# Performance work log

Measured on AMD Instinct MI355X. Metric: run time of the kernel, lower is better.

Reference implementation:

```python
import jax, jax.numpy as jnp
import numpy as np

N = 8192
IN_F = 512
OUT_F = 512
ALPHA = 0.2  # LeakyReLU negative slope
MASK_VAL = -9e15


def setup_inputs() -> dict:
    key = jax.random.key(0)
    k1, k2, k3, k4 = jax.random.split(key, 4)
    h = jax.random.normal(k1, (N, IN_F), dtype=jnp.float32)
    adj = jax.random.randint(k2, (N, N), 0, 2, dtype=jnp.int32)
    # Xavier-uniform-like init for params
    limW = float(1.414 * np.sqrt(6.0 / (IN_F + OUT_F)))
    W = jax.random.uniform(k3, (IN_F, OUT_F), dtype=jnp.float32, minval=-limW, maxval=limW)
    lima = float(1.414 * np.sqrt(6.0 / (2 * OUT_F + 1)))
    a = jax.random.uniform(k4, (2 * OUT_F, 1), dtype=jnp.float32, minval=-lima, maxval=lima)
    return {"h": h, "adj": adj, "W": W, "a": a}


def reference(h, adj, W, a):
    Wh = h @ W                                   # [N, F_out]
    a1 = a[:OUT_F, 0]                            # [F_out]
    a2 = a[OUT_F:, 0]                            # [F_out]
    # e_ij = leakyrelu(Wh_i . a1 + Wh_j . a2), broadcast sum instead of concat
    e = jax.nn.leaky_relu((Wh @ a1)[:, None] + (Wh @ a2)[None, :], negative_slope=ALPHA)
    attention = jnp.where(adj > 0, e, MASK_VAL)  # [N, N]
    attention = jax.nn.softmax(attention, axis=1)
    similarity = attention                       # softmax=True branch
    h_prime = attention @ Wh                     # [N, F_out]
    return jax.nn.elu(h_prime), similarity       # concat=True branch
```

## Files before the change

### kernel.cpp

```cpp
#include <hip/hip_runtime.h>
#include <stdint.h>
#include <stddef.h>

#define NN 8192
#define FD 512
#define ATTN_OFF (NN * FD)

typedef __attribute__((ext_vector_type(8))) short bf16x8;
typedef __attribute__((ext_vector_type(4))) float f32x4;
typedef __attribute__((ext_vector_type(4))) int i32x4;
typedef __attribute__((ext_vector_type(2))) uint32_t u32x2;
typedef __attribute__((ext_vector_type(4))) uint32_t u32x4;
typedef __attribute__((ext_vector_type(4))) uint16_t u16x4;

static __device__ __forceinline__ uint16_t f2bf(float x){
    union { float f; uint32_t u; } v; v.f = x;
    uint32_t r = v.u + 0x7FFFu + ((v.u >> 16) & 1u);
    return (uint16_t)(r >> 16);
}

#define GLDS(gp, lp) \
    __builtin_amdgcn_global_load_lds((__attribute__((address_space(1))) void*)(gp), \
                                     (__attribute__((address_space(3))) void*)(lp), 16, 0, 0)

__global__ void k_va(const float* __restrict__ W, const float* __restrict__ a,
                     float* __restrict__ va1, float* __restrict__ va2){
    const int lane = threadIdx.x & 63, wave = threadIdx.x >> 6;
    const int k = blockIdx.x*8 + wave;
    const float* wr = W + (size_t)k*FD;
    float s1 = 0.f, s2 = 0.f;
    #pragma unroll
    for (int e = 0; e < 2; ++e){
        int c = e*256 + lane*4;
        f32x4 wv = *(const f32x4*)(wr + c);
        f32x4 x1 = *(const f32x4*)(a + c);
        f32x4 x2 = *(const f32x4*)(a + FD + c);
        s1 += wv[0]*x1[0] + wv[1]*x1[1] + wv[2]*x1[2] + wv[3]*x1[3];
        s2 += wv[0]*x2[0] + wv[1]*x2[1] + wv[2]*x2[2] + wv[3]*x2[3];
    }
    for (int off = 32; off; off >>= 1){ s1 += __shfl_down(s1, off); s2 += __shfl_down(s2, off); }
    if (lane == 0){ va1[k] = s1; va2[k] = s2; }
}

__global__ void k_convW(const float* __restrict__ W, uint16_t* __restrict__ WT_b){
    int idx = blockIdx.x * 256 + threadIdx.x;
    for (int i = idx; i < FD*FD; i += 256*256){
        int n = i >> 9, k = i & 511;
        WT_b[i] = f2bf(W[(size_t)k*FD + n]);
    }
}

__global__ void k_rows(const float* __restrict__ h, const float* __restrict__ va1,
                       const float* __restrict__ va2, uint16_t* __restrict__ h_b,
                       float* __restrict__ Tarr,
                       float* __restrict__ E1p, float* __restrict__ E1n,
                       float* __restrict__ E2p, float* __restrict__ E2n){
    const int lane = threadIdx.x & 63, wave = threadIdx.x >> 6;
    const int row = blockIdx.x*4 + wave;
    const float* hr = h + (size_t)row * FD;
    float s1 = 0.f, s2 = 0.f;
    #pragma unroll
    for (int e = 0; e < 2; ++e){
        int c = e*256 + lane*4;
        f32x4 hv = *(const f32x4*)(hr + c);
        f32x4 x1 = *(const f32x4*)(va1 + c);
        f32x4 x2 = *(const f32x4*)(va2 + c);
        s1 += hv[0]*x1[0] + hv[1]*x1[1] + hv[2]*x1[2] + hv[3]*x1[3];
        s2 += hv[0]*x2[0] + hv[1]*x2[1] + hv[2]*x2[2] + hv[3]*x2[3];
        u16x4 o;
        o[0]=f2bf(hv[0]); o[1]=f2bf(hv[1]); o[2]=f2bf(hv[2]); o[3]=f2bf(hv[3]);
        *(u16x4*)(h_b + (size_t)row*FD + c) = o;
    }
    for (int off = 32; off; off >>= 1){ s1 += __shfl_down(s1, off); s2 += __shfl_down(s2, off); }
    if (lane == 0){
        Tarr[row] = expf(-s1);
        E1p[row]  = expf(s1);
        E1n[row]  = expf(0.2f*s1);
        E2p[row]  = expf(s2);
        E2n[row]  = expf(0.2f*s2);
    }
}

__global__ void k_pack(const int* __restrict__ adj, const float* __restrict__ Tarr,
                       const float* __restrict__ E1p, const float* __restrict__ E1n,
                       const float* __restrict__ E2p, const float* __restrict__ E2n,
                       uint32_t* __restrict__ packed, float* __restrict__ rowP,
                       float* __restrict__ rowN){
    extern __shared__ char smem[];
    float* P_s = (float*)smem;
    float* Q_s = (float*)(smem + 32768);
    const int tid = threadIdx.x, lane = tid & 63, wave = tid >> 6;
    for (int t = tid; t < NN/4; t += 256){
        ((f32x4*)P_s)[t] = ((const f32x4*)E2p)[t];
        ((f32x4*)Q_s)[t] = ((const f32x4*)E2n)[t];
    }
    __syncthreads();
    const int row = blockIdx.x*4 + wave;
    const float T_i = Tarr[row];
    const int* arow = adj + (size_t)row * NN;
    float Ap = 0.f, An = 0.f;
    #pragma unroll
    for (int g = 0; g < 4; ++g){
        uint32_t word = 0;
        #pragma unroll
        for (int e = 0; e < 8; ++e){
            int j0 = g*2048 + e*256 + lane*4;
            i32x4 av = __builtin_nontemporal_load((const i32x4*)(arow + j0));
            f32x4 p = ((const f32x4*)P_s)[j0 >> 2];
            f32x4 q = ((const f32x4*)Q_s)[j0 >> 2];
            #pragma unroll
            for (int c = 0; c < 4; ++c){
                if (av[c] != 0){
                    if (p[c] > T_i) Ap += p[c]; else An += q[c];
                    word |= (1u << (e*4 + c));
                }
            }
        }
        packed[(size_t)row*256 + g*64 + lane] = word;
    }
    #pragma unroll
    for (int off = 32; off; off >>= 1){
        Ap += __shfl_xor(Ap, off);
        An += __shfl_xor(An, off);
    }
    if (lane == 0){
        float e1p = E1p[row], e1n = E1n[row];
        float inv = 1.0f / (e1p*Ap + e1n*An);
        rowP[row] = e1p * inv;
        rowN[row] = e1n * inv;
    }
}

static __device__ __forceinline__ void mfma_tile(const char* A_base, const char* B_base,
                                                 int wave, int lane, f32x4 acc[2][4]){
    #pragma unroll
    for (int kk = 0; kk < 2; ++kk){
        bf16x8 afr[2], bfr[4];
        #pragma unroll
        for (int t = 0; t < 2; ++t){
            int rowl = t*16 + (lane & 15);
            int slot = (kk*4 + (lane >> 4)) ^ (rowl & 7);
            afr[t] = *(const bf16x8*)(A_base + rowl*128 + slot*16);
        }
        #pragma unroll
        for (int n = 0; n < 4; ++n){
            int nl = wave*64 + n*16 + (lane & 15);
            int slot = (kk*4 + (lane >> 4)) ^ (nl & 7);
            bfr[n] = *(const bf16x8*)(B_base + nl*128 + slot*16);
        }
        #pragma unroll
        for (int t = 0; t < 2; ++t)
            #pragma unroll
            for (int n = 0; n < 4; ++n)
                acc[t][n] = __builtin_amdgcn_mfma_f32_16x16x32_bf16(afr[t], bfr[n], acc[t][n], 0, 0, 0);
    }
}

__global__ __launch_bounds__(512) void k_wh(const uint16_t* __restrict__ h_b,
                                            const uint16_t* __restrict__ WT_b,
                                            uint16_t* __restrict__ WhbT){
    extern __shared__ char smem[];
    char* A_base = smem;
    char* B_base = smem + 4096;
    const int tid = threadIdx.x, wave = tid >> 6, lane = tid & 63;
    const int mb0 = blockIdx.x * 32;
    f32x4 acc[2][4];
    #pragma unroll
    for (int t = 0; t < 2; ++t)
        #pragma unroll
        for (int n = 0; n < 4; ++n) acc[t][n] = (f32x4){0.f,0.f,0.f,0.f};

    for (int k0 = 0; k0 < FD; k0 += 64){
        if (wave < 4){
            int m = wave*8 + (lane >> 3);
            int chunk = (lane & 7) ^ (m & 7);
            GLDS(h_b + (size_t)(mb0 + m)*FD + k0 + chunk*8, A_base + wave*1024);
        }
        #pragma unroll
        for (int r = 0; r < 8; ++r){
            int nn = wave*64 + r*8 + (lane >> 3);
            int chunk = (lane & 7) ^ (nn & 7);
            GLDS(WT_b + (size_t)nn*FD + k0 + chunk*8, B_base + (wave*64 + r*8)*128);
        }
        __syncthreads();
        mfma_tile(A_base, B_base, wave, lane, acc);
        __syncthreads();
    }
    uint16_t* Ts = (uint16_t*)B_base;
    #pragma unroll
    for (int t = 0; t < 2; ++t)
        #pragma unroll
        for (int n = 0; n < 4; ++n)
            #pragma unroll
            for (int r = 0; r < 4; ++r){
                int nl = wave*64 + n*16 + (lane & 15);
                int m  = t*16 + (lane >> 4)*4 + r;
                Ts[nl*40 + m] = f2bf(acc[t][n][r]);
            }
    __syncthreads();
    {
        int n = tid;
        const u32x4* src = (const u32x4*)(Ts + n*40);
        u32x4* dst = (u32x4*)(WhbT + (size_t)n*NN + mb0);
        #pragma unroll
        for (int r = 0; r < 4; ++r) dst[r] = src[r];
    }
}

__global__ __launch_bounds__(512) void k_gemm(const uint32_t* __restrict__ packed,
                                              const uint16_t* __restrict__ WhbT,
                                              const float* __restrict__ Tarr,
                                              const float* __restrict__ rowP,
                                              const float* __restrict__ rowN,
                                              const float* __restrict__ E2p,
                                              const float* __restrict__ E2n,
                                              float* __restrict__ hp_part,
                                              float* __restrict__ out){
    extern __shared__ char smem[];
    char* A_lds = smem;
    char* B_lds = smem + 16384;

    const int tid = threadIdx.x, wave = tid >> 6, lane = tid & 63;
    const int il = tid >> 3, jg = tid & 7;
    const int bi = blockIdx.x;
    const int ks = (bi & 7) >> 1;
    const int m_idx = (bi >> 3)*2 + (bi & 1);
    const int row0 = m_idx * 128;
    const int kbase = ks * 2048;

    float Tv[2], rPv[2], rNv[2];
    #pragma unroll
    for (int s = 0; s < 2; ++s){
        int gr = row0 + il + 64*s;
        Tv[s] = Tarr[gr]; rPv[s] = rowP[gr]; rNv[s] = rowN[gr];
    }

    f32x4 acc[8][4];
    #pragma unroll
    for (int mi = 0; mi < 8; ++mi)
        #pragma unroll
        for (int n = 0; n < 4; ++n) acc[mi][n] = (f32x4){0.f,0.f,0.f,0.f};

    auto BLOAD = [&](int t, u32x4 br[4]){
        const int k0 = kbase + t*32;
        #pragma unroll
        for (int rr = 0; rr < 4; ++rr){
            int n  = wave*64 + rr*16 + (lane >> 2);
            int cg = lane & 3;
            br[rr] = *(const u32x4*)(WhbT + (size_t)n*NN + k0 + cg*8);
        }
    };
    auto GEN = [&](int t, uint32_t aw[2][2]){
        const int k0 = kbase + t*32;
        f32x4 p = *(const f32x4*)(E2p + k0 + jg*4);
        f32x4 q = *(const f32x4*)(E2n + k0 + jg*4);
        const int widx  = ks*64 + (t & 7)*8 + jg;
        const int shift = ((t >> 3) & 7)*4;
        #pragma unroll
        for (int s = 0; s < 2; ++s){
            int grow = row0 + il + 64*s;
            uint32_t word = packed[(size_t)grow*256 + widx];
            float va[4];
            #pragma unroll
            for (int c = 0; c < 4; ++c){
                float val = (p[c] > Tv[s]) ? rPv[s]*p[c] : rNv[s]*q[c];
                va[c] = ((word >> (shift + c)) & 1u) ? val : 0.f;
            }
            f32x4 st; st[0]=va[0]; st[1]=va[1]; st[2]=va[2]; st[3]=va[3];
            __builtin_nontemporal_store(st, (f32x4*)(out + ATTN_OFF + (size_t)grow*NN + k0 + jg*4));
            aw[s][0] = ((uint32_t)f2bf(va[1]) << 16) | f2bf(va[0]);
            aw[s][1] = ((uint32_t)f2bf(va[3]) << 16) | f2bf(va[2]);
        }
    };
    auto WRITE_LDS = [&](int side, uint32_t aw[2][2], u32x4 br[4]){
        char* A = A_lds + side*8192;
        char* B = B_lds + side*32768;
        #pragma unroll
        for (int s = 0; s < 2; ++s){
            int rowl = il + 64*s;
            int addr = rowl*64 + (((jg >> 1) ^ (rowl & 3)) << 4) + ((jg & 1) << 3);
            u32x2 w; w[0] = aw[s][0]; w[1] = aw[s][1];
            *(u32x2*)(A + addr) = w;
        }
        #pragma unroll
        for (int rr = 0; rr < 4; ++rr){
            int n  = wave*64 + rr*16 + (lane >> 2);
            int cg = lane & 3;
            *(u32x4*)(B + n*64 + ((cg ^ (n & 3)) << 4)) = br[rr];
        }
    };

    {
        uint32_t aw[2][2]; u32x4 br[4];
        BLOAD(0, br); GEN(0, aw);
        WRITE_LDS(0, aw, br);
        asm volatile("s_waitcnt lgkmcnt(0)" ::: "memory");
        __builtin_amdgcn_s_barrier();
    }

    for (int t = 0; t < 64; ++t){
        uint32_t aw[2][2]; u32x4 br[4];
        if (t < 63){ BLOAD(t+1, br); GEN(t+1, aw); }
        {
            const char* A = A_lds + (t & 1)*8192;
            const char* B = B_lds + (t & 1)*32768;
            bf16x8 afr[8], bfr[4];
            #pragma unroll
            for (int mi = 0; mi < 8; ++mi){
                int rowl = mi*16 + (lane & 15);
                afr[mi] = *(const bf16x8*)(A + rowl*64 + (((lane >> 4) ^ (rowl & 3)) << 4));
            }
            #pragma unroll
            for (int nf = 0; nf < 4; ++nf){
                int nl = wave*64 + nf*16 + (lane & 15);
                bfr[nf] = *(const bf16x8*)(B + nl*64 + (((lane >> 4) ^ (nl & 3)) << 4));
            }
            __builtin_amdgcn_s_setprio(1);
            #pragma unroll
            for (int mi = 0; mi < 8; ++mi)
                #pragma unroll
                for (int nf = 0; nf < 4; ++nf)
                    acc[mi][nf] = __builtin_amdgcn_mfma_f32_16x16x32_bf16(afr[mi], bfr[nf], acc[mi][nf], 0, 0, 0);
            __builtin_amdgcn_s_setprio(0);
        }
        if (t < 63){
            WRITE_LDS((t+1) & 1, aw, br);
            asm volatile("s_waitcnt lgkmcnt(0)" ::: "memory");
            __builtin_amdgcn_s_barrier();
        }
    }
    float* hp = hp_part + (size_t)ks * NN * FD;
    #pragma unroll
    for (int mi = 0; mi < 8; ++mi)
        #pragma unroll
        for (int n = 0; n < 4; ++n)
            #pragma unroll
            for (int r = 0; r < 4; ++r){
                int m   = row0 + mi*16 + (lane >> 4)*4 + r;
                int col = wave*64 + n*16 + (lane & 15);
                hp[(size_t)m*FD + col] = acc[mi][n][r];
            }
}

__global__ __launch_bounds__(512) void k_red(const float* __restrict__ hp,
                                             float* __restrict__ out){
    const size_t i = (size_t)blockIdx.x * 512 + threadIdx.x;
    const size_t off = (size_t)NN * FD / 4;
    f32x4 a = ((const f32x4*)hp)[i];
    f32x4 b = ((const f32x4*)hp)[i + off];
    f32x4 c = ((const f32x4*)hp)[i + off*2];
    f32x4 d = ((const f32x4*)hp)[i + off*3];
    f32x4 s;
    #pragma unroll
    for (int e = 0; e < 4; ++e){
        float x = (a[e] + b[e]) + (c[e] + d[e]);
        s[e] = (x > 0.f) ? x : expm1f(x);
    }
    ((f32x4*)out)[i] = s;
}

extern "C" void kernel_launch(void* const* d_in, const int* in_sizes, int n_in,
                              void* d_out, int out_size, void* d_ws, size_t ws_size,
                              hipStream_t stream){
    (void)in_sizes; (void)n_in; (void)out_size; (void)ws_size;
    const float* h   = (const float*)d_in[0];
    const int*   adj = (const int*)  d_in[1];
    const float* W   = (const float*)d_in[2];
    const float* a   = (const float*)d_in[3];
    float* out = (float*)d_out;

    char* ws = (char*)d_ws;
    uint16_t* WhbT   = (uint16_t*)(ws);
    uint16_t* h_b    = (uint16_t*)(ws + (8u<<20));
    uint32_t* packed = (uint32_t*)(ws + (8u<<20));
    uint16_t* WT_b   = (uint16_t*)(ws + (16u<<20));
    float* fb   = (float*)(ws + (17u<<20));
    float* va1  = fb;            float* va2  = fb + 512;
    float* Tarr = fb + 1024;
    float* E1p  = Tarr + NN;     float* E1n  = E1p + NN;
    float* E2p  = E1n + NN;      float* E2n  = E2p + NN;
    float* rowP = E2n + NN;      float* rowN = rowP + NN;
    float* hp_part = (float*)(ws + (32u<<20));

    hipFuncSetAttribute((const void*)k_pack, hipFuncAttributeMaxDynamicSharedMemorySize, 65536);
    hipFuncSetAttribute((const void*)k_wh,   hipFuncAttributeMaxDynamicSharedMemorySize, 69632);
    hipFuncSetAttribute((const void*)k_gemm, hipFuncAttributeMaxDynamicSharedMemorySize, 81920);

    k_va   <<<64,   512, 0,      stream>>>(W, a, va1, va2);
    k_rows <<<2048, 256, 0,      stream>>>(h, va1, va2, h_b, Tarr, E1p, E1n, E2p, E2n);
    k_convW<<<256,  256, 0,      stream>>>(W, WT_b);
    k_wh   <<<256,  512, 69632,  stream>>>(h_b, WT_b, WhbT);
    k_pack <<<2048, 256, 65536,  stream>>>(adj, Tarr, E1p, E1n, E2p, E2n, packed, rowP, rowN);
    k_gemm <<<256,  512, 81920,  stream>>>(packed, WhbT, Tarr, rowP, rowN, E2p, E2n, hp_part, out);
    k_red  <<<2048, 512, 0,      stream>>>(hp_part, out);
}
```

Before: 245.5 us.

## Fuse adjacency packing and softmax denominators into the attention GEMM kernel

The separate k_pack kernel is removed. Each k_main block now reads its own 128x2048 adjacency slice, builds ballot bitmasks in LDS, and adds partial softmax denominators to global memory with atomics. The four K-split blocks of a row tile then meet at a global-counter spin barrier before normalising. This drops one launch and the packed bitmask round trip through global memory. In exchange it adds atomics, a spin wait that relies on all four blocks being resident at once, and more LDS per block, which may reduce occupancy.

Result: slower. 255.8 us (+4.2%).

```diff
diff --git a/kernel.cpp b/kernel.cpp
--- a/kernel.cpp
+++ b/kernel.cpp
@@ -24,9 +24,14 @@
                                      (__attribute__((address_space(3))) void*)(lp), 16, 0, 0)
 
 __global__ void k_va(const float* __restrict__ W, const float* __restrict__ a,
-                     float* __restrict__ va1, float* __restrict__ va2){
+                     float* __restrict__ va1, float* __restrict__ va2,
+                     float* __restrict__ denomP, float* __restrict__ denomN,
+                     int* __restrict__ counter){
     const int lane = threadIdx.x & 63, wave = threadIdx.x >> 6;
     const int k = blockIdx.x*8 + wave;
+    const int gidx = blockIdx.x*512 + threadIdx.x;
+    if (gidx < NN){ denomP[gidx] = 0.f; denomN[gidx] = 0.f; }
+    if (gidx < 64) counter[gidx] = 0;
     const float* wr = W + (size_t)k*FD;
     float s1 = 0.f, s2 = 0.f;
     #pragma unroll
@@ -81,56 +86,6 @@
     }
 }
 
-__global__ void k_pack(const int* __restrict__ adj, const float* __restrict__ Tarr,
-                       const float* __restrict__ E1p, const float* __restrict__ E1n,
-                       const float* __restrict__ E2p, const float* __restrict__ E2n,
-                       uint32_t* __restrict__ packed, float* __restrict__ rowP,
-                       float* __restrict__ rowN){
-    extern __shared__ char smem[];
-    float* P_s = (float*)smem;
-    float* Q_s = (float*)(smem + 32768);
-    const int tid = threadIdx.x, lane = tid & 63, wave = tid >> 6;
-    for (int t = tid; t < NN/4; t += 256){
-        ((f32x4*)P_s)[t] = ((const f32x4*)E2p)[t];
-        ((f32x4*)Q_s)[t] = ((const f32x4*)E2n)[t];
-    }
-    __syncthreads();
-    const int row = blockIdx.x*4 + wave;
-    const float T_i = Tarr[row];
-    const int* arow = adj + (size_t)row * NN;
-    float Ap = 0.f, An = 0.f;
-    #pragma unroll
-    for (int g = 0; g < 4; ++g){
-        uint32_t word = 0;
-        #pragma unroll
-        for (int e = 0; e < 8; ++e){
-            int j0 = g*2048 + e*256 + lane*4;
-            i32x4 av = __builtin_nontemporal_load((const i32x4*)(arow + j0));
-            f32x4 p = ((const f32x4*)P_s)[j0 >> 2];
-            f32x4 q = ((const f32x4*)Q_s)[j0 >> 2];
-            #pragma unroll
-            for (int c = 0; c < 4; ++c){
-                if (av[c] != 0){
-                    if (p[c] > T_i) Ap += p[c]; else An += q[c];
-                    word |= (1u << (e*4 + c));
-                }
-            }
-        }
-        packed[(size_t)row*256 + g*64 + lane] = word;
-    }
-    #pragma unroll
-    for (int off = 32; off; off >>= 1){
-        Ap += __shfl_xor(Ap, off);
-        An += __shfl_xor(An, off);
-    }
-    if (lane == 0){
-        float e1p = E1p[row], e1n = E1n[row];
-        float inv = 1.0f / (e1p*Ap + e1n*An);
-        rowP[row] = e1p * inv;
-        rowN[row] = e1n * inv;
-    }
-}
-
 static __device__ __forceinline__ void mfma_tile(const char* A_base, const char* B_base,
                                                  int wave, int lane, f32x4 acc[2][4]){
     #pragma unroll
@@ -207,18 +162,25 @@
     }
 }
 
-__global__ __launch_bounds__(512) void k_gemm(const uint32_t* __restrict__ packed,
+__global__ __launch_bounds__(512) void k_main(const int* __restrict__ adj,
                                               const uint16_t* __restrict__ WhbT,
                                               const float* __restrict__ Tarr,
-                                              const float* __restrict__ rowP,
-                                              const float* __restrict__ rowN,
+                                              const float* __restrict__ E1p,
+                                              const float* __restrict__ E1n,
                                               const float* __restrict__ E2p,
                                               const float* __restrict__ E2n,
+                                              float* __restrict__ denomP,
+                                              float* __restrict__ denomN,
+                                              int* __restrict__ counter,
                                               float* __restrict__ hp_part,
                                               float* __restrict__ out){
     extern __shared__ char smem[];
-    char* A_lds = smem;
-    char* B_lds = smem + 16384;
+    uint64_t* pk   = (uint64_t*)smem;
+    float* T_s     = (float*)(smem + 33792);
+    float* rP_s    = (float*)(smem + 34304);
+    float* rN_s    = (float*)(smem + 34816);
+    char*  A_lds   = smem + 35328;
+    char*  B_lds   = smem + 51712;
 
     const int tid = threadIdx.x, wave = tid >> 6, lane = tid & 63;
     const int il = tid >> 3, jg = tid & 7;
@@ -228,11 +190,59 @@
     const int row0 = m_idx * 128;
     const int kbase = ks * 2048;
 
+    for (int rr = 0; rr < 16; ++rr){
+        const int rloc = wave*16 + rr;
+        const int grow = row0 + rloc;
+        const int* arow = adj + (size_t)grow*NN + kbase;
+        const float T_i = Tarr[grow];
+        float Ap = 0.f, An = 0.f;
+        #pragma unroll
+        for (int e = 0; e < 8; ++e){
+            i32x4 av = __builtin_nontemporal_load((const i32x4*)(arow + e*256 + lane*4));
+            f32x4 p = *(const f32x4*)(E2p + kbase + e*256 + lane*4);
+            f32x4 q = *(const f32x4*)(E2n + kbase + e*256 + lane*4);
+            #pragma unroll
+            for (int c = 0; c < 4; ++c){
+                if (av[c] != 0){ if (p[c] > T_i) Ap += p[c]; else An += q[c]; }
+            }
+            uint64_t b0 = __ballot(av[0] != 0);
+            uint64_t b1 = __ballot(av[1] != 0);
+            uint64_t b2 = __ballot(av[2] != 0);
+            uint64_t b3 = __ballot(av[3] != 0);
+            if (lane == 0){
+                uint64_t* d = pk + rloc*33 + e*4;
+                d[0] = b0; d[1] = b1; d[2] = b2; d[3] = b3;
+            }
+        }
+        #pragma unroll
+        for (int off = 32; off; off >>= 1){
+            Ap += __shfl_xor(Ap, off);
+            An += __shfl_xor(An, off);
+        }
+        if (lane == 0){ atomicAdd(denomP + grow, Ap); atomicAdd(denomN + grow, An); }
+    }
+    __syncthreads();
+    if (tid == 0){
+        __threadfence();
+        atomicAdd(counter + m_idx, 1);
+        while (atomicAdd(counter + m_idx, 0) < 4) __builtin_amdgcn_s_sleep(2);
+    }
+    __syncthreads();
+    if (tid < 128){
+        const int grow = row0 + tid;
+        float sAp = atomicAdd(denomP + grow, 0.0f);
+        float sAn = atomicAdd(denomN + grow, 0.0f);
+        float e1p = E1p[grow], e1n = E1n[grow];
+        float inv = 1.0f / (e1p*sAp + e1n*sAn);
+        rP_s[tid] = e1p*inv; rN_s[tid] = e1n*inv; T_s[tid] = Tarr[grow];
+    }
+    __syncthreads();
+
     float Tv[2], rPv[2], rNv[2];
     #pragma unroll
     for (int s = 0; s < 2; ++s){
-        int gr = row0 + il + 64*s;
-        Tv[s] = Tarr[gr]; rPv[s] = rowP[gr]; rNv[s] = rowN[gr];
+        int rl = il + 64*s;
+        Tv[s] = T_s[rl]; rPv[s] = rP_s[rl]; rNv[s] = rN_s[rl];
     }
 
     f32x4 acc[8][4];
@@ -254,17 +264,18 @@
         const int k0 = kbase + t*32;
         f32x4 p = *(const f32x4*)(E2p + k0 + jg*4);
         f32x4 q = *(const f32x4*)(E2n + k0 + jg*4);
-        const int widx  = ks*64 + (t & 7)*8 + jg;
-        const int shift = ((t >> 3) & 7)*4;
+        const int ebase = (t >> 3)*4;
+        const int bidx  = (t & 7)*8 + jg;
         #pragma unroll
         for (int s = 0; s < 2; ++s){
-            int grow = row0 + il + 64*s;
-            uint32_t word = packed[(size_t)grow*256 + widx];
+            const int rl = il + 64*s;
+            const int grow = row0 + rl;
+            const uint64_t* pw = pk + rl*33 + ebase;
             float va[4];
             #pragma unroll
             for (int c = 0; c < 4; ++c){
                 float val = (p[c] > Tv[s]) ? rPv[s]*p[c] : rNv[s]*q[c];
-                va[c] = ((word >> (shift + c)) & 1u) ? val : 0.f;
+                va[c] = ((pw[c] >> bidx) & 1ull) ? val : 0.f;
             }
             f32x4 st; st[0]=va[0]; st[1]=va[1]; st[2]=va[2]; st[3]=va[3];
             __builtin_nontemporal_store(st, (f32x4*)(out + ATTN_OFF + (size_t)grow*NN + k0 + jg*4));
@@ -297,7 +308,6 @@
         asm volatile("s_waitcnt lgkmcnt(0)" ::: "memory");
         __builtin_amdgcn_s_barrier();
     }
-
     for (int t = 0; t < 64; ++t){
         uint32_t aw[2][2]; u32x4 br[4];
         if (t < 63){ BLOAD(t+1, br); GEN(t+1, aw); }
@@ -372,25 +382,24 @@
     char* ws = (char*)d_ws;
     uint16_t* WhbT   = (uint16_t*)(ws);
     uint16_t* h_b    = (uint16_t*)(ws + (8u<<20));
-    uint32_t* packed = (uint32_t*)(ws + (8u<<20));
     uint16_t* WT_b   = (uint16_t*)(ws + (16u<<20));
     float* fb   = (float*)(ws + (17u<<20));
     float* va1  = fb;            float* va2  = fb + 512;
     float* Tarr = fb + 1024;
     float* E1p  = Tarr + NN;     float* E1n  = E1p + NN;
     float* E2p  = E1n + NN;      float* E2n  = E2p + NN;
-    float* rowP = E2n + NN;      float* rowN = rowP + NN;
+    float* denomP = E2n + NN;    float* denomN = denomP + NN;
+    int*   counter = (int*)(denomN + NN);
     float* hp_part = (float*)(ws + (32u<<20));
 
-    hipFuncSetAttribute((const void*)k_pack, hipFuncAttributeMaxDynamicSharedMemorySize, 65536);
     hipFuncSetAttribute((const void*)k_wh,   hipFuncAttributeMaxDynamicSharedMemorySize, 69632);
-    hipFuncSetAttribute((const void*)k_gemm, hipFuncAttributeMaxDynamicSharedMemorySize, 81920);
-
-    k_va   <<<64,   512, 0,      stream>>>(W, a, va1, va2);
+    hipFuncSetAttribute((const void*)k_main, hipFuncAttributeMaxDynamicSharedMemorySize, 117248);
+
+    k_va   <<<64,   512, 0,      stream>>>(W, a, va1, va2, denomP, denomN, counter);
     k_rows <<<2048, 256, 0,      stream>>>(h, va1, va2, h_b, Tarr, E1p, E1n, E2p, E2n);
     k_convW<<<256,  256, 0,      stream>>>(W, WT_b);
     k_wh   <<<256,  512, 69632,  stream>>>(h_b, WT_b, WhbT);
-    k_pack <<<2048, 256, 65536,  stream>>>(adj, Tarr, E1p, E1n, E2p, E2n, packed, rowP, rowN);
-    k_gemm <<<256,  512, 81920,  stream>>>(packed, WhbT, Tarr, rowP, rowN, E2p, E2n, hp_part, out);
+    k_main <<<256,  512, 117248, stream>>>(adj, WhbT, Tarr, E1p, E1n, E2p, E2n,
+                                           denomP, denomN, counter, hp_part, out);
     k_red  <<<2048, 512, 0,      stream>>>(hp_part, out);
 }
```

## Split attention-matrix write into separate kernel and pipeline GEMM B loads via LDS DMA

Applied to the files above, without the earlier changes.

Moves the 256MB attention-matrix store out of the GEMM into a dedicated streaming kernel (k_write). The GEMM now triple-buffers B tiles with global_load_lds, preloads the packed mask words into registers, and stages E2p/E2n in LDS. The aim is to keep the MFMA loop from stalling on the large nontemporal stores and register-staged loads. In exchange it adds an extra launch, rereads the packed mask and row scalars, moves packed to its own workspace region, and raises LDS use to 128KB, which limits occupancy.

Result: slower. 290.5 us (+18.3%).

```diff
diff --git a/kernel.cpp b/kernel.cpp
--- a/kernel.cpp
+++ b/kernel.cpp
@@ -131,6 +131,57 @@
     }
 }
 
+__global__ __launch_bounds__(256) void k_write(
+        const uint32_t* __restrict__ packed, const float* __restrict__ Tarr,
+        const float* __restrict__ rowP, const float* __restrict__ rowN,
+        const float* __restrict__ E2p, const float* __restrict__ E2n,
+        float* __restrict__ out){
+    const int tid = threadIdx.x;
+    const int jslice = blockIdx.x & 7;
+    const int rchunk = blockIdx.x >> 3;
+    const int j  = jslice*1024 + tid*4;
+    const int r0 = rchunk*64;
+    const int widx  = (j >> 11)*64 + ((j >> 2) & 63);
+    const int shift = ((j >> 8) & 7) * 4;
+    const f32x4 p = *(const f32x4*)(E2p + j);
+    const f32x4 q = *(const f32x4*)(E2n + j);
+    float* obase = out + ATTN_OFF + j;
+
+    uint32_t wA[16]; float tA[16], pA[16], nA[16];
+    #pragma unroll
+    for (int i = 0; i < 16; ++i){
+        int row = r0 + i;
+        wA[i] = packed[(size_t)row*256 + widx];
+        tA[i] = Tarr[row]; pA[i] = rowP[row]; nA[i] = rowN[row];
+    }
+    for (int rb = 0; rb < 4; ++rb){
+        uint32_t wB[16]; float tB[16], pB[16], nB[16];
+        if (rb < 3){
+            #pragma unroll
+            for (int i = 0; i < 16; ++i){
+                int row = r0 + (rb+1)*16 + i;
+                wB[i] = packed[(size_t)row*256 + widx];
+                tB[i] = Tarr[row]; pB[i] = rowP[row]; nB[i] = rowN[row];
+            }
+        }
+        __builtin_amdgcn_sched_barrier(0);
+        #pragma unroll
+        for (int i = 0; i < 16; ++i){
+            int row = r0 + rb*16 + i;
+            f32x4 st;
+            #pragma unroll
+            for (int c = 0; c < 4; ++c){
+                float val = (p[c] > tA[i]) ? pA[i]*p[c] : nA[i]*q[c];
+                st[c] = ((wA[i] >> (shift + c)) & 1u) ? val : 0.f;
+            }
+            __builtin_nontemporal_store(st, (f32x4*)(obase + (size_t)row*NN));
+        }
+        __builtin_amdgcn_sched_barrier(0);
+        #pragma unroll
+        for (int i = 0; i < 16; ++i){ wA[i]=wB[i]; tA[i]=tB[i]; pA[i]=pB[i]; nA[i]=nB[i]; }
+    }
+}
+
 static __device__ __forceinline__ void mfma_tile(const char* A_base, const char* B_base,
                                                  int wave, int lane, f32x4 acc[2][4]){
     #pragma unroll
@@ -214,11 +265,12 @@
                                               const float* __restrict__ rowN,
                                               const float* __restrict__ E2p,
                                               const float* __restrict__ E2n,
-                                              float* __restrict__ hp_part,
-                                              float* __restrict__ out){
+                                              float* __restrict__ hp_part){
     extern __shared__ char smem[];
-    char* A_lds = smem;
-    char* B_lds = smem + 16384;
+    float* E2P_s = (float*)smem;
+    float* E2N_s = (float*)(smem + 8192);
+    char*  A_lds = smem + 16384;
+    char*  B_lds = smem + 32768;
 
     const int tid = threadIdx.x, wave = tid >> 6, lane = tid & 63;
     const int il = tid >> 3, jg = tid & 7;
@@ -234,6 +286,15 @@
         int gr = row0 + il + 64*s;
         Tv[s] = Tarr[gr]; rPv[s] = rowP[gr]; rNv[s] = rowN[gr];
     }
+    uint32_t wds0[8], wds1[8];
+    #pragma unroll
+    for (int w = 0; w < 8; ++w){
+        wds0[w] = packed[(size_t)(row0 + il     )*256 + ks*64 + w*8 + jg];
+        wds1[w] = packed[(size_t)(row0 + il + 64)*256 + ks*64 + w*8 + jg];
+    }
+    ((f32x4*)E2P_s)[tid] = ((const f32x4*)(E2p + kbase))[tid];
+    ((f32x4*)E2N_s)[tid] = ((const f32x4*)(E2n + kbase))[tid];
+    __syncthreads();
 
     f32x4 acc[8][4];
     #pragma unroll
@@ -241,94 +302,93 @@
         #pragma unroll
         for (int n = 0; n < 4; ++n) acc[mi][n] = (f32x4){0.f,0.f,0.f,0.f};
 
-    auto BLOAD = [&](int t, u32x4 br[4]){
+    auto STAGE_B = [&](int slot, int t){
+        char* Bb = B_lds + slot*32768;
         const int k0 = kbase + t*32;
         #pragma unroll
         for (int rr = 0; rr < 4; ++rr){
             int n  = wave*64 + rr*16 + (lane >> 2);
-            int cg = lane & 3;
-            br[rr] = *(const u32x4*)(WhbT + (size_t)n*NN + k0 + cg*8);
+            int cg = (lane & 3) ^ ((n >> 1) & 3);
+            GLDS(WhbT + (size_t)n*NN + k0 + cg*8, Bb + (wave*64 + rr*16)*64);
         }
     };
-    auto GEN = [&](int t, uint32_t aw[2][2]){
-        const int k0 = kbase + t*32;
-        f32x4 p = *(const f32x4*)(E2p + k0 + jg*4);
-        f32x4 q = *(const f32x4*)(E2n + k0 + jg*4);
-        const int widx  = ks*64 + (t & 7)*8 + jg;
-        const int shift = ((t >> 3) & 7)*4;
-        #pragma unroll
-        for (int s = 0; s < 2; ++s){
-            int grow = row0 + il + 64*s;
-            uint32_t word = packed[(size_t)grow*256 + widx];
-            float va[4];
-            #pragma unroll
-            for (int c = 0; c < 4; ++c){
-                float val = (p[c] > Tv[s]) ? rPv[s]*p[c] : rNv[s]*q[c];
-                va[c] = ((word >> (shift + c)) & 1u) ? val : 0.f;
-            }
-            f32x4 st; st[0]=va[0]; st[1]=va[1]; st[2]=va[2]; st[3]=va[3];
-            __builtin_nontemporal_store(st, (f32x4*)(out + ATTN_OFF + (size_t)grow*NN + k0 + jg*4));
-            aw[s][0] = ((uint32_t)f2bf(va[1]) << 16) | f2bf(va[0]);
-            aw[s][1] = ((uint32_t)f2bf(va[3]) << 16) | f2bf(va[2]);
-        }
+    auto MFMA_STEP = [&](int side, int slot){
+        const char* A = A_lds + side*8192;
+        const char* B = B_lds + slot*32768;
+        bf16x8 afr[8], bfr[4];
+        #pragma unroll
+        for (int mi = 0; mi < 8; ++mi){
+            int rowl = mi*16 + (lane & 15);
+            afr[mi] = *(const bf16x8*)(A + rowl*64 + (((lane >> 4) ^ (rowl & 3)) << 4));
+        }
+        #pragma unroll
+        for (int nf = 0; nf < 4; ++nf){
+            int nl = wave*64 + nf*16 + (lane & 15);
+            int slt = (lane >> 4) ^ ((nl >> 1) & 3);
+            bfr[nf] = *(const bf16x8*)(B + nl*64 + slt*16);
+        }
+        __builtin_amdgcn_s_setprio(1);
+        #pragma unroll
+        for (int mi = 0; mi < 8; ++mi)
+            #pragma unroll
+            for (int nf = 0; nf < 4; ++nf)
+                acc[mi][nf] = __builtin_amdgcn_mfma_f32_16x16x32_bf16(afr[mi], bfr[nf], acc[mi][nf], 0, 0, 0);
+        __builtin_amdgcn_s_setprio(0);
     };
-    auto WRITE_LDS = [&](int side, uint32_t aw[2][2], u32x4 br[4]){
-        char* A = A_lds + side*8192;
-        char* B = B_lds + side*32768;
-        #pragma unroll
-        for (int s = 0; s < 2; ++s){
-            int rowl = il + 64*s;
-            int addr = rowl*64 + (((jg >> 1) ^ (rowl & 3)) << 4) + ((jg & 1) << 3);
-            u32x2 w; w[0] = aw[s][0]; w[1] = aw[s][1];
-            *(u32x2*)(A + addr) = w;
-        }
-        #pragma unroll
-        for (int rr = 0; rr < 4; ++rr){
-            int n  = wave*64 + rr*16 + (lane >> 2);
-            int cg = lane & 3;
-            *(u32x4*)(B + n*64 + ((cg ^ (n & 3)) << 4)) = br[rr];
-        }
-    };
-
+
+    #define GEN_A(side, g8, w) {                                                       \
+        const int t_ = (g8)*8 + (w);                                                   \
+        f32x4 p = *(const f32x4*)(E2P_s + t_*32 + jg*4);                               \
+        f32x4 q = *(const f32x4*)(E2N_s + t_*32 + jg*4);                               \
+        const int shift_ = ((g8) & 7)*4;                                               \
+        char* A = A_lds + (side)*8192;                                                 \
+        uint32_t wv_[2] = { wds0[w], wds1[w] };                                        \
+        _Pragma("unroll")                                                              \
+        for (int s = 0; s < 2; ++s){                                                   \
+            float va[4];                                                               \
+            _Pragma("unroll")                                                          \
+            for (int c = 0; c < 4; ++c){                                               \
+                float val = (p[c] > Tv[s]) ? rPv[s]*p[c] : rNv[s]*q[c];                \
+                va[c] = ((wv_[s] >> (shift_ + c)) & 1u) ? val : 0.f;                   \
+            }                                                                          \
+            int rowl = il + 64*s;                                                      \
+            int addr = rowl*64 + (((jg >> 1) ^ (rowl & 3)) << 4) + ((jg & 1) << 3);    \
+            u32x2 wpk; wpk[0] = ((uint32_t)f2bf(va[1]) << 16) | f2bf(va[0]);           \
+            wpk[1] = ((uint32_t)f2bf(va[3]) << 16) | f2bf(va[2]);                      \
+            *(u32x2*)(A + addr) = wpk;                                                 \
+        }                                                                              \
+    }
+
+    STAGE_B(0, 0); STAGE_B(1, 1);
+    GEN_A(0, 0, 0);
+    asm volatile("s_waitcnt vmcnt(4) lgkmcnt(0)" ::: "memory");
+    __builtin_amdgcn_s_barrier();
+
+    for (int g8 = 0; g8 < 7; ++g8){
+        #pragma unroll
+        for (int w = 0; w < 8; ++w){
+            const int t = g8*8 + w;
+            STAGE_B((t+2)%3, t+2);
+            if (w < 7){ GEN_A((t+1)&1, g8, w+1); }
+            else      { GEN_A((t+1)&1, g8+1, 0); }
+            MFMA_STEP(t&1, t%3);
+            asm volatile("s_waitcnt vmcnt(4) lgkmcnt(0)" ::: "memory");
+            __builtin_amdgcn_s_barrier();
+        }
+    }
     {
-        uint32_t aw[2][2]; u32x4 br[4];
-        BLOAD(0, br); GEN(0, aw);
-        WRITE_LDS(0, aw, br);
-        asm volatile("s_waitcnt lgkmcnt(0)" ::: "memory");
-        __builtin_amdgcn_s_barrier();
-    }
-
-    for (int t = 0; t < 64; ++t){
-        uint32_t aw[2][2]; u32x4 br[4];
-        if (t < 63){ BLOAD(t+1, br); GEN(t+1, aw); }
-        {
-            const char* A = A_lds + (t & 1)*8192;
-            const char* B = B_lds + (t & 1)*32768;
-            bf16x8 afr[8], bfr[4];
-            #pragma unroll
-            for (int mi = 0; mi < 8; ++mi){
-                int rowl = mi*16 + (lane & 15);
-                afr[mi] = *(const bf16x8*)(A + rowl*64 + (((lane >> 4) ^ (rowl & 3)) << 4));
-            }
-            #pragma unroll
-            for (int nf = 0; nf < 4; ++nf){
-                int nl = wave*64 + nf*16 + (lane & 15);
-                bfr[nf] = *(const bf16x8*)(B + nl*64 + (((lane >> 4) ^ (nl & 3)) << 4));
-            }
-            __builtin_amdgcn_s_setprio(1);
-            #pragma unroll
-            for (int mi = 0; mi < 8; ++mi)
-                #pragma unroll
-                for (int nf = 0; nf < 4; ++nf)
-                    acc[mi][nf] = __builtin_amdgcn_mfma_f32_16x16x32_bf16(afr[mi], bfr[nf], acc[mi][nf], 0, 0, 0);
-            __builtin_amdgcn_s_setprio(0);
-        }
-        if (t < 63){
-            WRITE_LDS((t+1) & 1, aw, br);
-            asm volatile("s_waitcnt lgkmcnt(0)" ::: "memory");
+        #pragma unroll
+        for (int w = 0; w < 8; ++w){
+            const int t = 56 + w;
+            if (t + 2 < 64) STAGE_B((t+2)%3, t+2);
+            if (w < 7) GEN_A((t+1)&1, 7, w+1);
+            MFMA_STEP(t&1, t%3);
+            asm volatile("s_waitcnt vmcnt(0) lgkmcnt(0)" ::: "memory");
             __builtin_amdgcn_s_barrier();
         }
     }
+    #undef GEN_A
+
     float* hp = hp_part + (size_t)ks * NN * FD;
     #pragma unroll
     for (int mi = 0; mi < 8; ++mi)
@@ -372,9 +432,9 @@
     char* ws = (char*)d_ws;
     uint16_t* WhbT   = (uint16_t*)(ws);
     uint16_t* h_b    = (uint16_t*)(ws + (8u<<20));
-    uint32_t* packed = (uint32_t*)(ws + (8u<<20));
     uint16_t* WT_b   = (uint16_t*)(ws + (16u<<20));
-    float* fb   = (float*)(ws + (17u<<20));
+    uint32_t* packed = (uint32_t*)(ws + (17u<<20));
+    float* fb   = (float*)(ws + (25u<<20));
     float* va1  = fb;            float* va2  = fb + 512;
     float* Tarr = fb + 1024;
     float* E1p  = Tarr + NN;     float* E1n  = E1p + NN;
@@ -384,13 +444,14 @@
 
     hipFuncSetAttribute((const void*)k_pack, hipFuncAttributeMaxDynamicSharedMemorySize, 65536);
     hipFuncSetAttribute((const void*)k_wh,   hipFuncAttributeMaxDynamicSharedMemorySize, 69632);
-    hipFuncSetAttribute((const void*)k_gemm, hipFuncAttributeMaxDynamicSharedMemorySize, 81920);
+    hipFuncSetAttribute((const void*)k_gemm, hipFuncAttributeMaxDynamicSharedMemorySize, 131072);
 
     k_va   <<<64,   512, 0,      stream>>>(W, a, va1, va2);
     k_rows <<<2048, 256, 0,      stream>>>(h, va1, va2, h_b, Tarr, E1p, E1n, E2p, E2n);
     k_convW<<<256,  256, 0,      stream>>>(W, WT_b);
     k_wh   <<<256,  512, 69632,  stream>>>(h_b, WT_b, WhbT);
     k_pack <<<2048, 256, 65536,  stream>>>(adj, Tarr, E1p, E1n, E2p, E2n, packed, rowP, rowN);
-    k_gemm <<<256,  512, 81920,  stream>>>(packed, WhbT, Tarr, rowP, rowN, E2p, E2n, hp_part, out);
+    k_gemm <<<256,  512, 131072, stream>>>(packed, WhbT, Tarr, rowP, rowN, E2p, E2n, hp_part);
+    k_write<<<1024, 256, 0,      stream>>>(packed, Tarr, rowP, rowN, E2p, E2n, out);
     k_red  <<<2048, 512, 0,      stream>>>(hp_part, out);
 }
```
